# Kernel optimization log

Hardware: AMD Instinct MI355X
Metric: run time of the kernel (lower is better)

Reference implementation:

```python
import jax, jax.numpy as jnp
import numpy as np
import math

D = 768      # d_model
H = 12       # heads
DH = D // H  # per-head dim
HID = 3072   # ffn hidden
L = 6        # layers each for encoder/decoder
S = 1024     # encoder seq len
T = 1024     # decoder seq len
MAXLEN = 1024


def pos_encoding(d, length):
    # pe[pos, 2i] = sin(pos / scale**i), pe[pos, 2i+1] = cos(pos / scale**i), scale = 1000**(2/d)
    scale = 1000.0 ** (2.0 / d)
    inv = scale ** (-np.arange(d // 2, dtype=np.float64))
    ang = np.arange(length, dtype=np.float64)[:, None] * inv[None, :]
    pe = np.zeros((length, d), dtype=np.float32)
    pe[:, 0::2] = np.sin(ang)
    pe[:, 1::2] = np.cos(ang)
    return jnp.asarray(pe)


def setup_inputs() -> dict:
    key = jax.random.key(0)
    ks = iter(jax.random.split(key, 64))
    def nrm(shape, s=0.02):
        return jax.random.normal(next(ks), shape, dtype=jnp.float32) * s
    inp = {
        'xl': nrm((S, D), 1.0),
        'dl': nrm((T, D), 1.0),
        'pos_enc': pos_encoding(D, MAXLEN),
        # encoder params (stacked over L layers, heads stacked over H)
        'enc_wq': nrm((L, H, DH, D)), 'enc_wk': nrm((L, H, DH, D)), 'enc_wv': nrm((L, H, DH, D)),
        'enc_wo': nrm((L, D, D)), 'enc_bo': jnp.zeros((L, D), jnp.float32),
        'enc_ln_a': jnp.ones((L, 2, D), jnp.float32), 'enc_ln_b': jnp.zeros((L, 2, D), jnp.float32),
        'enc_w1': nrm((L, HID, D)), 'enc_b1': jnp.zeros((L, HID), jnp.float32),
        'enc_w2': nrm((L, D, HID)), 'enc_b2': jnp.zeros((L, D), jnp.float32),
        # decoder self-attention
        'dec_wq': nrm((L, H, DH, D)), 'dec_wk': nrm((L, H, DH, D)), 'dec_wv': nrm((L, H, DH, D)),
        'dec_wo': nrm((L, D, D)), 'dec_bo': jnp.zeros((L, D), jnp.float32),
        # decoder cross-attention
        'dec_cwq': nrm((L, H, DH, D)), 'dec_cwk': nrm((L, H, DH, D)), 'dec_cwv': nrm((L, H, DH, D)),
        'dec_cwo': nrm((L, D, D)), 'dec_cbo': jnp.zeros((L, D), jnp.float32),
        'dec_ln_a': jnp.ones((L, 3, D), jnp.float32), 'dec_ln_b': jnp.zeros((L, 3, D), jnp.float32),
        'dec_w1': nrm((L, HID, D)), 'dec_b1': jnp.zeros((L, HID), jnp.float32),
        'dec_w2': nrm((L, D, HID)), 'dec_b2': jnp.zeros((L, D), jnp.float32),
    }
    return inp


def _ln_res(x, fx, a, b, eps=1e-6):
    # x = x + fx; a*(x-mean)/(std+eps)+b with UNBIASED std (torch default) and std (not var) in denom
    x = x + fx
    m = x.mean(-1, keepdims=True)
    s = jnp.std(x, axis=-1, keepdims=True, ddof=1)
    return a * (x - m) / (s + eps) + b


def _mha(qx, kx, vx, wq, wk, wv, wo, bo, mask=None):
    q = jnp.einsum('sd,hed->hse', qx, wq)  # [H,S,dh]
    k = jnp.einsum('td,hed->hte', kx, wk)
    v = jnp.einsum('td,hed->hte', vx, wv)
    scores = jnp.einsum('hse,hte->hst', q, k) / math.sqrt(q.shape[-1])
    if mask is not None:
        scores = scores + mask
    p = jax.nn.softmax(scores, axis=-1)  # softmax over keys (torch dim=1 on 2D scores)
    o = jnp.einsum('hst,hte->hse', p, v)
    o = jnp.transpose(o, (1, 0, 2)).reshape(qx.shape[0], -1)  # concat heads
    return o @ wo.T + bo


def _ffn(x, w1, b1, w2, b2):
    return jax.nn.relu(x @ w1.T + b1) @ w2.T + b2


def reference(xl, dl, pos_enc, enc_wq, enc_wk, enc_wv, enc_wo, enc_bo, enc_ln_a, enc_ln_b,
              enc_w1, enc_b1, enc_w2, enc_b2,
              dec_wq, dec_wk, dec_wv, dec_wo, dec_bo,
              dec_cwq, dec_cwk, dec_cwv, dec_cwo, dec_cbo,
              dec_ln_a, dec_ln_b, dec_w1, dec_b1, dec_w2, dec_b2):
    m = xl + pos_enc[: xl.shape[0]]
    for l in range(L):
        fx = _mha(m, m, m, enc_wq[l], enc_wk[l], enc_wv[l], enc_wo[l], enc_bo[l])
        m = _ln_res(m, fx, enc_ln_a[l, 0], enc_ln_b[l, 0])
        fx = _ffn(m, enc_w1[l], enc_b1[l], enc_w2[l], enc_b2[l])
        m = _ln_res(m, fx, enc_ln_a[l, 1], enc_ln_b[l, 1])
    n = dl.shape[0]
    # additive causal mask: -10000 where j > i
    cmask = -10000.0 * (jnp.arange(n)[None, :] > jnp.arange(n)[:, None]).astype(jnp.float32)
    out = dl + pos_enc[:n]
    for l in range(L):
        fx = _mha(out, out, out, dec_wq[l], dec_wk[l], dec_wv[l], dec_wo[l], dec_bo[l], cmask)
        out = _ln_res(out, fx, dec_ln_a[l, 0], dec_ln_b[l, 0])
        fx = _mha(out, m, m, dec_cwq[l], dec_cwk[l], dec_cwv[l], dec_cwo[l], dec_cbo[l])
        out = _ln_res(out, fx, dec_ln_a[l, 1], dec_ln_b[l, 1])
        fx = _ffn(out, dec_w1[l], dec_b1[l], dec_w2[l], dec_b2[l])
        out = _ln_res(out, fx, dec_ln_a[l, 2], dec_ln_b[l, 2])
    return jax.nn.softmax(out, axis=1)
```

## Files before the change

### kernel.cpp

```cpp
#include <hip/hip_runtime.h>
#include <math.h>

#define DMODEL 768
#define NHEAD 12
#define DHEAD 64
#define HIDDEN 3072
#define NLAYER 6
#define SEQ 1024
#define AC_ELEMS (SEQ * DMODEL)

typedef unsigned short u16;
typedef __attribute__((ext_vector_type(8))) short short8;
typedef __attribute__((ext_vector_type(4))) float f32x4;

__device__ __forceinline__ u16 f2bf(float f) {
    union { float f; unsigned u; } v; v.f = f;
    unsigned u = v.u;
    return (u16)((u + 0x7fffu + ((u >> 16) & 1u)) >> 16);
}
__device__ __forceinline__ float bf2f(u16 b) {
    union { unsigned u; float f; } v; v.u = ((unsigned)b) << 16; return v.f;
}

__device__ __forceinline__ void async16(const void* g, void* l) {
    __builtin_amdgcn_global_load_lds(
        (const __attribute__((address_space(1))) unsigned int*)g,
        (__attribute__((address_space(3))) unsigned int*)l, 16, 0, 0);
}

__device__ __forceinline__ float block_sum(float v, float* red) {
    int tid = threadIdx.x;
    red[tid] = v;
    __syncthreads();
#pragma unroll
    for (int s = 128; s > 0; s >>= 1) {
        if (tid < s) red[tid] += red[tid + s];
        __syncthreads();
    }
    float r = red[0];
    __syncthreads();
    return r;
}
__device__ __forceinline__ float block_max(float v, float* red) {
    int tid = threadIdx.x;
    red[tid] = v;
    __syncthreads();
#pragma unroll
    for (int s = 128; s > 0; s >>= 1) {
        if (tid < s) red[tid] = fmaxf(red[tid], red[tid + s]);
        __syncthreads();
    }
    float r = red[0];
    __syncthreads();
    return r;
}

__global__ __launch_bounds__(256) void add_pe(const float* __restrict__ a,
                                              const float* __restrict__ b,
                                              float* __restrict__ o,
                                              u16* __restrict__ ob, int n) {
    int i = blockIdx.x * 256 + threadIdx.x;
    if (i < n) { float v = a[i] + b[i]; o[i] = v; ob[i] = f2bf(v); }
}

__global__ __launch_bounds__(256) void cvt_bf16(const float* __restrict__ src,
                                                u16* __restrict__ dst,
                                                long long per, long long sls, long long dls) {
    long long i = ((long long)blockIdx.x * 256 + threadIdx.x) * 4;
    if (i >= per) return;
    const float* s = src + (long long)blockIdx.y * sls + i;
    u16* d = dst + (long long)blockIdx.y * dls + i;
    float4 v = *(const float4*)s;
    ushort4 o;
    o.x = f2bf(v.x); o.y = f2bf(v.y); o.z = f2bf(v.z); o.w = f2bf(v.w);
    *(ushort4*)d = o;
}

template<int TM, int TN, int WR, int WC>
__global__ __launch_bounds__(WR * WC * 64) void gemm_mfma(
    const u16* __restrict__ A, int lda,
    const void* __restrict__ Bp, int ldb, int b_f32,
    const float* __restrict__ bias,
    void* __restrict__ Cp, int ldc, int c_bf16,
    float* __restrict__ C2,
    u16* __restrict__ vt_out, int vt_col0,
    int Ksub, int relu)
{
    constexpr int T  = WR * WC * 64;
    constexpr int FM = TM / (WR * 16), FN = TN / (WC * 16);
    constexpr int NA = TM * 8 / T, NB = TN * 8 / T;
    __shared__ __align__(16) u16 As[2][TM * 64];
    __shared__ __align__(16) u16 Bs[2][TN * 64];

    const int zs = blockIdx.z;
    const u16*   B16 = (const u16*)Bp   + (long long)zs * Ksub;
    const float* B32 = (const float*)Bp + (long long)zs * Ksub;
    A += (long long)zs * Ksub;
    u16*   C16 = (u16*)Cp;
    float* C32 = (float*)Cp;

    const int t = threadIdx.x, lane = t & 63, w = t >> 6;
    const int wy = w / WC, wx = w % WC;
    const int n0 = blockIdx.y * TM, m0 = blockIdx.x * TN;

    auto stage = [&](int b, int k0) {
#pragma unroll
        for (int i = 0; i < NA; ++i) {
            int L = i * T + t;
            int row = L >> 3, cp = L & 7, c = cp ^ (row & 7);
            async16(A + (long long)(n0 + row) * lda + k0 + (c << 3),
                    &As[b][(i * T + w * 64) * 8]);
        }
        if (!b_f32) {
#pragma unroll
            for (int i = 0; i < NB; ++i) {
                int L = i * T + t;
                int row = L >> 3, cp = L & 7, c = cp ^ (row & 7);
                async16(B16 + (long long)(m0 + row) * ldb + k0 + (c << 3),
                        &Bs[b][(i * T + w * 64) * 8]);
            }
        } else {
#pragma unroll
            for (int i = 0; i < NB; ++i) {
                int L = i * T + t;
                int row = L >> 3, cp = L & 7, c = cp ^ (row & 7);
                const float* s = B32 + (long long)(m0 + row) * ldb + k0 + (c << 3);
                float4 x = *(const float4*)s;
                float4 y = *(const float4*)(s + 4);
                uint4 pk;
                pk.x = (unsigned)f2bf(x.x) | ((unsigned)f2bf(x.y) << 16);
                pk.y = (unsigned)f2bf(x.z) | ((unsigned)f2bf(x.w) << 16);
                pk.z = (unsigned)f2bf(y.x) | ((unsigned)f2bf(y.y) << 16);
                pk.w = (unsigned)f2bf(y.z) | ((unsigned)f2bf(y.w) << 16);
                *(uint4*)&Bs[b][row * 64 + cp * 8] = pk;
            }
        }
    };

    const int nk = Ksub / 64;
    stage(0, 0);
    __syncthreads();

    f32x4 acc[FM][FN] = {};

    for (int tt = 0; tt < nk; ++tt) {
        const int cur = tt & 1;
        if (tt + 1 < nk) stage(cur ^ 1, (tt + 1) * 64);

        const u16* Ac = As[cur];
        const u16* Bc = Bs[cur];
#pragma unroll
        for (int kk = 0; kk < 2; ++kk) {
            short8 af[FM], bfv[FN];
            const int cb = kk * 4 + (lane >> 4);
#pragma unroll
            for (int m = 0; m < FM; ++m) {
                int R = wy * (TM / WR) + m * 16 + (lane & 15);
                af[m] = *(const short8*)&Ac[R * 64 + ((cb ^ (R & 7)) << 3)];
            }
#pragma unroll
            for (int n = 0; n < FN; ++n) {
                int R = wx * (TN / WC) + n * 16 + (lane & 15);
                bfv[n] = *(const short8*)&Bc[R * 64 + ((cb ^ (R & 7)) << 3)];
            }
#pragma unroll
            for (int m = 0; m < FM; ++m)
#pragma unroll
                for (int n = 0; n < FN; ++n)
                    acc[m][n] = __builtin_amdgcn_mfma_f32_16x16x32_bf16(af[m], bfv[n], acc[m][n], 0, 0, 0);
        }
        __syncthreads();
    }

    const int cj = lane & 15, ci0 = (lane >> 4) << 2;
    const bool z0 = (zs == 0);
#pragma unroll
    for (int m = 0; m < FM; ++m) {
#pragma unroll
        for (int n = 0; n < FN; ++n) {
            int col = m0 + wx * (TN / WC) + n * 16 + cj;
            bool to_vt = z0 && vt_out && (col >= vt_col0);
            float bv = (z0 && bias) ? bias[col] : 0.0f;
#pragma unroll
            for (int r = 0; r < 4; ++r) {
                int row = n0 + wy * (TM / WR) + m * 16 + ci0 + r;
                float v = acc[m][n][r] + bv;
                if (relu) v = fmaxf(v, 0.0f);
                if (!z0)          C2[(long long)row * ldc + col] = v;
                else if (to_vt)   vt_out[(long long)(col - vt_col0) * SEQ + row] = f2bf(v);
                else if (c_bf16)  C16[(long long)row * ldc + col] = f2bf(v);
                else              C32[(long long)row * ldc + col] = v;
            }
        }
    }
}

template<int CAUSAL>
__global__ __launch_bounds__(256) void attn_split(
    const u16* __restrict__ Qg,
    const u16* __restrict__ Kg,
    const u16* __restrict__ VT,
    float* __restrict__ Op,
    float* __restrict__ Ml)
{
    const int h  = blockIdx.y;
    const int qt = blockIdx.x;
    const int s  = blockIdx.z;
    const int q0 = qt * 64;
    const int t = threadIdx.x, lane = t & 63, w = t >> 6;

    const int last = CAUSAL ? qt : (SEQ / 64 - 1);

    if (CAUSAL && s > last) {
        for (int e = t; e < 64 * 64; e += 256) {
            int r = e >> 6, c = e & 63;
            Op[(long long)s * AC_ELEMS + (long long)(q0 + r) * DMODEL + h * 64 + c] = 0.0f;
        }
        if (t < 64) {
            long long mi = (((long long)s * NHEAD + h) * SEQ + q0 + t) * 2;
            Ml[mi] = -3.0e38f; Ml[mi + 1] = 0.0f;
        }
        return;
    }

    __shared__ __align__(16) u16 Ks[2][64 * 64];
    __shared__ __align__(16) u16 Vs[2][64 * 64];
    __shared__ __align__(16) u16 Ps[4][16 * 64];

    short8 qf[2];
    {
        int qrow = q0 + w * 16 + (lane & 15);
        const u16* qp = Qg + (long long)qrow * (3 * DMODEL) + h * DHEAD + ((lane >> 4) << 3);
        qf[0] = *(const short8*)qp;
        qf[1] = *(const short8*)(qp + 32);
    }

    auto stage = [&](int b, int kt) {
#pragma unroll
        for (int i = 0; i < 2; ++i) {
            int LL = i * 256 + t;
            int row = LL >> 3, cp = LL & 7, c = cp ^ (row & 7);
            async16(Kg + (long long)(kt * 64 + row) * (3 * DMODEL) + h * DHEAD + (c << 3),
                    &Ks[b][(i * 256 + w * 64) * 8]);
            async16(VT + (long long)(h * DHEAD + row) * SEQ + kt * 64 + (c << 3),
                    &Vs[b][(i * 256 + w * 64) * 8]);
        }
    };

    f32x4 o_acc[4] = {};
    float m_r[4], l_r[4];
#pragma unroll
    for (int r = 0; r < 4; ++r) { m_r[r] = -3.0e38f; l_r[r] = 0.f; }

    stage(0, s);
    __syncthreads();

    int buf = 0;
    for (int kt = s; kt <= last; kt += 2) {
        if (kt + 2 <= last) stage(buf ^ 1, kt + 2);

        f32x4 sv[4] = {};
#pragma unroll
        for (int kk = 0; kk < 2; ++kk) {
            const int cb = kk * 4 + (lane >> 4);
#pragma unroll
            for (int n = 0; n < 4; ++n) {
                int R = n * 16 + (lane & 15);
                short8 kf = *(const short8*)&Ks[buf][R * 64 + ((cb ^ (R & 7)) << 3)];
                sv[n] = __builtin_amdgcn_mfma_f32_16x16x32_bf16(qf[kk], kf, sv[n], 0, 0, 0);
            }
        }

#pragma unroll
        for (int n = 0; n < 4; ++n) {
            int keyl = n * 16 + (lane & 15);
#pragma unroll
            for (int r = 0; r < 4; ++r) {
                float v = sv[n][r] * 0.125f;
                if (CAUSAL && kt == qt) {
                    int ql = w * 16 + ((lane >> 4) << 2) + r;
                    if (keyl > ql) v -= 10000.0f;
                }
                sv[n][r] = v;
            }
        }

#pragma unroll
        for (int r = 0; r < 4; ++r) {
            float vm = fmaxf(fmaxf(sv[0][r], sv[1][r]), fmaxf(sv[2][r], sv[3][r]));
            vm = fmaxf(vm, __shfl_xor(vm, 1));
            vm = fmaxf(vm, __shfl_xor(vm, 2));
            vm = fmaxf(vm, __shfl_xor(vm, 4));
            vm = fmaxf(vm, __shfl_xor(vm, 8));
            float mn = fmaxf(m_r[r], vm);
            float sf = __expf(m_r[r] - mn);
            m_r[r] = mn;
            float rowsum = 0.f;
#pragma unroll
            for (int n = 0; n < 4; ++n) {
                float p = __expf(sv[n][r] - mn);
                sv[n][r] = p;
                rowsum += p;
            }
            rowsum += __shfl_xor(rowsum, 1);
            rowsum += __shfl_xor(rowsum, 2);
            rowsum += __shfl_xor(rowsum, 4);
            rowsum += __shfl_xor(rowsum, 8);
            l_r[r] = l_r[r] * sf + rowsum;
#pragma unroll
            for (int d = 0; d < 4; ++d) o_acc[d][r] *= sf;
        }

#pragma unroll
        for (int n = 0; n < 4; ++n) {
            int jh = lane & 7;
            int chunk = n * 2 + ((lane & 15) >> 3);
#pragma unroll
            for (int r = 0; r < 4; ++r) {
                int q = ((lane >> 4) << 2) + r;
                Ps[w][q * 64 + ((chunk ^ (q & 7)) << 3) + jh] = f2bf(sv[n][r]);
            }
        }

#pragma unroll
        for (int kk = 0; kk < 2; ++kk) {
            int q = lane & 15;
            int chunk = (lane >> 4) + kk * 4;
            short8 pf = *(const short8*)&Ps[w][q * 64 + ((chunk ^ (q & 7)) << 3)];
            const int cb = kk * 4 + (lane >> 4);
#pragma unroll
            for (int d = 0; d < 4; ++d) {
                int R = d * 16 + (lane & 15);
                short8 vf = *(const short8*)&Vs[buf][R * 64 + ((cb ^ (R & 7)) << 3)];
                o_acc[d] = __builtin_amdgcn_mfma_f32_16x16x32_bf16(pf, vf, o_acc[d], 0, 0, 0);
            }
        }
        __syncthreads();
        buf ^= 1;
    }

#pragma unroll
    for (int r = 0; r < 4; ++r) {
        int row = q0 + w * 16 + ((lane >> 4) << 2) + r;
#pragma unroll
        for (int d = 0; d < 4; ++d) {
            int col = h * DHEAD + d * 16 + (lane & 15);
            Op[(long long)s * AC_ELEMS + (long long)row * DMODEL + col] = o_acc[d][r];
        }
        if ((lane & 15) == 0) {
            long long mi = (((long long)s * NHEAD + h) * SEQ + row) * 2;
            Ml[mi] = m_r[r]; Ml[mi + 1] = l_r[r];
        }
    }
}

__global__ __launch_bounds__(192) void attn_combine(const float* __restrict__ Op,
                                                    const float* __restrict__ Ml,
                                                    u16* __restrict__ O) {
    const int row = blockIdx.x;
    const int c0 = threadIdx.x * 4;
    const int h = c0 >> 6;
    long long m0i = (((long long)0 * NHEAD + h) * SEQ + row) * 2;
    long long m1i = (((long long)1 * NHEAD + h) * SEQ + row) * 2;
    float m0 = Ml[m0i], l0 = Ml[m0i + 1];
    float m1 = Ml[m1i], l1 = Ml[m1i + 1];
    float M = fmaxf(m0, m1);
    float w0 = __expf(m0 - M), w1 = __expf(m1 - M);
    float inv = 1.0f / (w0 * l0 + w1 * l1);
    float4 a = *(const float4*)&Op[(long long)row * DMODEL + c0];
    float4 b = *(const float4*)&Op[(long long)AC_ELEMS + (long long)row * DMODEL + c0];
    ushort4 o;
    o.x = f2bf((w0 * a.x + w1 * b.x) * inv);
    o.y = f2bf((w0 * a.y + w1 * b.y) * inv);
    o.z = f2bf((w0 * a.z + w1 * b.z) * inv);
    o.w = f2bf((w0 * a.w + w1 * b.w) * inv);
    *(ushort4*)&O[(long long)row * DMODEL + c0] = o;
}

__global__ __launch_bounds__(256) void softmax_f32(const float* __restrict__ in,
                                                   float* __restrict__ out, int width) {
    const float* row = in + (long long)blockIdx.x * width;
    float* orow = out + (long long)blockIdx.x * width;
    int tid = threadIdx.x;
    __shared__ float red[256];
    int nf4 = width >> 2;
    float4 v = {-1e30f, -1e30f, -1e30f, -1e30f};
    if (tid < nf4) v = ((const float4*)row)[tid];
    float mx = fmaxf(fmaxf(v.x, v.y), fmaxf(v.z, v.w));
    mx = block_max(mx, red);
    float4 e = {0.f, 0.f, 0.f, 0.f};
    float s = 0.f;
    if (tid < nf4) {
        e.x = __expf(v.x - mx); e.y = __expf(v.y - mx);
        e.z = __expf(v.z - mx); e.w = __expf(v.w - mx);
        s = e.x + e.y + e.z + e.w;
    }
    s = block_sum(s, red);
    float inv = 1.0f / s;
    if (tid < nf4) {
        e.x *= inv; e.y *= inv; e.z *= inv; e.w *= inv;
        ((float4*)orow)[tid] = e;
    }
}

__global__ __launch_bounds__(256) void ln_res_kernel(float* __restrict__ x,
                                                     const float* __restrict__ fx,
                                                     const float* __restrict__ fx2,
                                                     const float* __restrict__ ga,
                                                     const float* __restrict__ gb,
                                                     u16* __restrict__ xb) {
    long long row = blockIdx.x;
    float* xr = x + row * DMODEL;
    const float* fr = fx + row * DMODEL;
    u16* xbr = xb + row * DMODEL;
    int tid = threadIdx.x;
    __shared__ float red[256];

    float4 tv = {0.f, 0.f, 0.f, 0.f};
    if (tid < 192) {
        float4 a = ((const float4*)xr)[tid];
        float4 f = ((const float4*)fr)[tid];
        tv.x = a.x + f.x; tv.y = a.y + f.y; tv.z = a.z + f.z; tv.w = a.w + f.w;
        if (fx2) {
            float4 g = ((const float4*)(fx2 + row * DMODEL))[tid];
            tv.x += g.x; tv.y += g.y; tv.z += g.z; tv.w += g.w;
        }
    }
    float sum = tv.x + tv.y + tv.z + tv.w;
    sum = block_sum(sum, red);
    float mean = sum * (1.0f / (float)DMODEL);

    float4 d = {0.f, 0.f, 0.f, 0.f};
    float ss = 0.f;
    if (tid < 192) {
        d.x = tv.x - mean; d.y = tv.y - mean; d.z = tv.z - mean; d.w = tv.w - mean;
        ss = d.x * d.x + d.y * d.y + d.z * d.z + d.w * d.w;
    }
    ss = block_sum(ss, red);
    float stdv = sqrtf(ss / (float)(DMODEL - 1));
    float inv = 1.0f / (stdv + 1e-6f);

    if (tid < 192) {
        float4 A = ((const float4*)ga)[tid];
        float4 B = ((const float4*)gb)[tid];
        float4 o;
        o.x = A.x * d.x * inv + B.x;
        o.y = A.y * d.y * inv + B.y;
        o.z = A.z * d.z * inv + B.z;
        o.w = A.w * d.w * inv + B.w;
        ((float4*)xr)[tid] = o;
        ushort4 ob;
        ob.x = f2bf(o.x); ob.y = f2bf(o.y); ob.z = f2bf(o.z); ob.w = f2bf(o.w);
        ((ushort4*)xbr)[tid] = ob;
    }
}

struct GArg {
    const u16* A; int lda;
    const void* B; int ldb; int b_f32;
    const float* bias;
    void* C; int ldc; int c_bf16;
    u16* vt; int vt_col0;
    int N, M, K; int relu;
};
template<int TM, int TN, int WR, int WC>
static inline void glaunch(hipStream_t st, const GArg& a, int splitk = 1, float* C2 = nullptr) {
    dim3 grid(a.M / TN, a.N / TM, splitk);
    hipLaunchKernelGGL((gemm_mfma<TM, TN, WR, WC>), grid, dim3(WR * WC * 64), 0, st,
                       a.A, a.lda, a.B, a.ldb, a.b_f32, a.bias, a.C, a.ldc, a.c_bf16,
                       C2, a.vt, a.vt_col0, a.K / splitk, a.relu);
}

extern "C" void kernel_launch(void* const* d_in, const int* in_sizes, int n_in,
                              void* d_out, int out_size, void* d_ws, size_t ws_size,
                              hipStream_t stream) {
    const float* xl      = (const float*)d_in[0];
    const float* dl      = (const float*)d_in[1];
    const float* pe      = (const float*)d_in[2];
    const float* enc_wq  = (const float*)d_in[3];
    const float* enc_wk  = (const float*)d_in[4];
    const float* enc_wv  = (const float*)d_in[5];
    const float* enc_wo  = (const float*)d_in[6];
    const float* enc_bo  = (const float*)d_in[7];
    const float* enc_lna = (const float*)d_in[8];
    const float* enc_lnb = (const float*)d_in[9];
    const float* enc_w1  = (const float*)d_in[10];
    const float* enc_b1  = (const float*)d_in[11];
    const float* enc_w2  = (const float*)d_in[12];
    const float* enc_b2  = (const float*)d_in[13];
    const float* dec_wq  = (const float*)d_in[14];
    const float* dec_wk  = (const float*)d_in[15];
    const float* dec_wv  = (const float*)d_in[16];
    const float* dec_wo  = (const float*)d_in[17];
    const float* dec_bo  = (const float*)d_in[18];
    const float* dec_cwq = (const float*)d_in[19];
    const float* dec_cwk = (const float*)d_in[20];
    const float* dec_cwv = (const float*)d_in[21];
    const float* dec_cwo = (const float*)d_in[22];
    const float* dec_cbo = (const float*)d_in[23];
    const float* dec_lna = (const float*)d_in[24];
    const float* dec_lnb = (const float*)d_in[25];
    const float* dec_w1  = (const float*)d_in[26];
    const float* dec_b1  = (const float*)d_in[27];
    const float* dec_w2  = (const float*)d_in[28];
    const float* dec_b2  = (const float*)d_in[29];

    const long long AC   = AC_ELEMS;
    const long long DD   = (long long)DMODEL * DMODEL;
    const long long WH   = (long long)HIDDEN * DMODEL;
    const long long QKVC = (long long)SEQ * 3 * DMODEL;
    const long long SH   = (long long)SEQ * HIDDEN;

    float* mbuf  = (float*)d_ws;
    float* xbuf  = mbuf + AC;
    float* fbuf  = xbuf + AC;
    float* fbuf2 = fbuf + AC;
    float* Opart = fbuf2 + AC;
    float* Ml    = Opart + 2 * AC;
    u16* u = (u16*)(Ml + 2LL * NHEAD * SEQ * 2);
    u16* mb16 = u;  u += AC;
    u16* xb16 = u;  u += AC;
    u16* qkvb = u;  u += QKVC;
    u16* vt   = u;  u += AC;
    u16* ob   = u;  u += AC;
    u16* hb   = u;  u += SH;

    u16* W = u;
    long long woff = 0;
    const long long W_ENC_QKV = woff; woff += 18 * DD;
    const long long W_ENC_WO  = woff; woff += 6 * DD;
    const long long W_ENC_W1  = woff; woff += 6 * WH;
    const long long W_ENC_W2  = woff; woff += 6 * WH;
    const long long W_DEC_QKV = woff; woff += 18 * DD;
    const long long W_DEC_CQKV= woff; woff += 18 * DD;
    const long long W_DEC_WO  = woff; woff += 6 * DD;
    const long long W_DEC_CWO = woff; woff += 6 * DD;
    const long long W_DEC_W1  = woff; woff += 6 * WH;
    const long long W_DEC_W2  = woff; woff += 6 * WH;
    const long long need = (long long)((char*)(W + woff) - (char*)d_ws);
    const bool conv = ((long long)ws_size >= need);

    if (conv) {
        auto cvt = [&](const float* src, long long dst_off, long long per, long long sls, long long dls, int L) {
            dim3 grid((unsigned)((per / 4 + 255) / 256), L);
            hipLaunchKernelGGL(cvt_bf16, grid, dim3(256), 0, stream, src, W + dst_off, per, sls, dls);
        };
        cvt(enc_wq, W_ENC_QKV + 0 * DD, DD, DD, 3 * DD, NLAYER);
        cvt(enc_wk, W_ENC_QKV + 1 * DD, DD, DD, 3 * DD, NLAYER);
        cvt(enc_wv, W_ENC_QKV + 2 * DD, DD, DD, 3 * DD, NLAYER);
        cvt(enc_wo, W_ENC_WO, 6 * DD, 0, 0, 1);
        cvt(enc_w1, W_ENC_W1, 6 * WH, 0, 0, 1);
        cvt(enc_w2, W_ENC_W2, 6 * WH, 0, 0, 1);
        cvt(dec_wq, W_DEC_QKV + 0 * DD, DD, DD, 3 * DD, NLAYER);
        cvt(dec_wk, W_DEC_QKV + 1 * DD, DD, DD, 3 * DD, NLAYER);
        cvt(dec_wv, W_DEC_QKV + 2 * DD, DD, DD, 3 * DD, NLAYER);
        cvt(dec_cwq, W_DEC_CQKV + 0 * DD, DD, DD, 3 * DD, NLAYER);
        cvt(dec_cwk, W_DEC_CQKV + 1 * DD, DD, DD, 3 * DD, NLAYER);
        cvt(dec_cwv, W_DEC_CQKV + 2 * DD, DD, DD, 3 * DD, NLAYER);
        cvt(dec_wo, W_DEC_WO, 6 * DD, 0, 0, 1);
        cvt(dec_cwo, W_DEC_CWO, 6 * DD, 0, 0, 1);
        cvt(dec_w1, W_DEC_W1, 6 * WH, 0, 0, 1);
        cvt(dec_w2, W_DEC_W2, 6 * WH, 0, 0, 1);
    }

    hipLaunchKernelGGL(add_pe, dim3((int)(AC / 256)), dim3(256), 0, stream, xl, pe, mbuf, mb16, (int)AC);

    auto attn = [&](int causal) {
        dim3 grid(SEQ / 64, NHEAD, 2);
        if (causal)
            hipLaunchKernelGGL((attn_split<1>), grid, dim3(256), 0, stream,
                               qkvb, qkvb + DMODEL, vt, Opart, Ml);
        else
            hipLaunchKernelGGL((attn_split<0>), grid, dim3(256), 0, stream,
                               qkvb, qkvb + DMODEL, vt, Opart, Ml);
        hipLaunchKernelGGL(attn_combine, dim3(SEQ), dim3(192), 0, stream, Opart, Ml, ob);
    };

    for (int l = 0; l < NLAYER; ++l) {
        if (conv) {
            GArg qkv = { mb16, DMODEL, W + W_ENC_QKV + l * 3 * DD, DMODEL, 0, nullptr,
                         qkvb, 3 * DMODEL, 1, vt, 2 * DMODEL, SEQ, 3 * DMODEL, DMODEL, 0 };
            glaunch<64, 64, 2, 2>(stream, qkv);
        } else {
            const float* wps[3] = { enc_wq + l * DD, enc_wk + l * DD, enc_wv + l * DD };
            for (int j = 0; j < 3; ++j) {
                GArg a = { mb16, DMODEL, wps[j], DMODEL, 1, nullptr,
                           qkvb + j * DMODEL, 3 * DMODEL, 1,
                           (j == 2) ? vt : nullptr, 0, SEQ, DMODEL, DMODEL, 0 };
                glaunch<32, 32, 1, 1>(stream, a);
            }
        }
        attn(0);
        GArg wo = { ob, DMODEL,
                    conv ? (const void*)(W + W_ENC_WO + l * DD) : (const void*)(enc_wo + l * DD),
                    DMODEL, conv ? 0 : 1, enc_bo + (long long)l * DMODEL,
                    fbuf, DMODEL, 0, nullptr, 0, SEQ, DMODEL, DMODEL, 0 };
        glaunch<32, 32, 1, 1>(stream, wo);
        hipLaunchKernelGGL(ln_res_kernel, dim3(SEQ), dim3(256), 0, stream,
                           mbuf, fbuf, (const float*)nullptr,
                           enc_lna + (long long)(l * 2 + 0) * DMODEL,
                           enc_lnb + (long long)(l * 2 + 0) * DMODEL, mb16);
        GArg f1 = { mb16, DMODEL,
                    conv ? (const void*)(W + W_ENC_W1 + l * WH) : (const void*)(enc_w1 + l * WH),
                    DMODEL, conv ? 0 : 1, enc_b1 + (long long)l * HIDDEN,
                    hb, HIDDEN, 1, nullptr, 0, SEQ, HIDDEN, DMODEL, 1 };
        glaunch<64, 64, 2, 2>(stream, f1);
        GArg f2 = { hb, HIDDEN,
                    conv ? (const void*)(W + W_ENC_W2 + l * WH) : (const void*)(enc_w2 + l * WH),
                    HIDDEN, conv ? 0 : 1, enc_b2 + (long long)l * DMODEL,
                    fbuf, DMODEL, 0, nullptr, 0, SEQ, DMODEL, HIDDEN, 0 };
        glaunch<64, 64, 2, 2>(stream, f2, 2, fbuf2);
        hipLaunchKernelGGL(ln_res_kernel, dim3(SEQ), dim3(256), 0, stream,
                           mbuf, fbuf, fbuf2,
                           enc_lna + (long long)(l * 2 + 1) * DMODEL,
                           enc_lnb + (long long)(l * 2 + 1) * DMODEL, mb16);
    }

    hipLaunchKernelGGL(add_pe, dim3((int)(AC / 256)), dim3(256), 0, stream, dl, pe, xbuf, xb16, (int)AC);

    for (int l = 0; l < NLAYER; ++l) {
        if (conv) {
            GArg qkv = { xb16, DMODEL, W + W_DEC_QKV + l * 3 * DD, DMODEL, 0, nullptr,
                         qkvb, 3 * DMODEL, 1, vt, 2 * DMODEL, SEQ, 3 * DMODEL, DMODEL, 0 };
            glaunch<64, 64, 2, 2>(stream, qkv);
        } else {
            const float* wps[3] = { dec_wq + l * DD, dec_wk + l * DD, dec_wv + l * DD };
            for (int j = 0; j < 3; ++j) {
                GArg a = { xb16, DMODEL, wps[j], DMODEL, 1, nullptr,
                           qkvb + j * DMODEL, 3 * DMODEL, 1,
                           (j == 2) ? vt : nullptr, 0, SEQ, DMODEL, DMODEL, 0 };
                glaunch<32, 32, 1, 1>(stream, a);
            }
        }
        attn(1);
        GArg wo = { ob, DMODEL,
                    conv ? (const void*)(W + W_DEC_WO + l * DD) : (const void*)(dec_wo + l * DD),
                    DMODEL, conv ? 0 : 1, dec_bo + (long long)l * DMODEL,
                    fbuf, DMODEL, 0, nullptr, 0, SEQ, DMODEL, DMODEL, 0 };
        glaunch<32, 32, 1, 1>(stream, wo);
        hipLaunchKernelGGL(ln_res_kernel, dim3(SEQ), dim3(256), 0, stream,
                           xbuf, fbuf, (const float*)nullptr,
                           dec_lna + (long long)(l * 3 + 0) * DMODEL,
                           dec_lnb + (long long)(l * 3 + 0) * DMODEL, xb16);

        if (conv) {
            GArg q = { xb16, DMODEL, W + W_DEC_CQKV + l * 3 * DD, DMODEL, 0, nullptr,
                       qkvb, 3 * DMODEL, 1, nullptr, 0, SEQ, DMODEL, DMODEL, 0 };
            glaunch<32, 32, 1, 1>(stream, q);
            GArg kv = { mb16, DMODEL, W + W_DEC_CQKV + l * 3 * DD + DD, DMODEL, 0, nullptr,
                        qkvb + DMODEL, 3 * DMODEL, 1, vt, DMODEL, SEQ, 2 * DMODEL, DMODEL, 0 };
            glaunch<32, 32, 1, 1>(stream, kv);
        } else {
            GArg q = { xb16, DMODEL, dec_cwq + l * DD, DMODEL, 1, nullptr,
                       qkvb, 3 * DMODEL, 1, nullptr, 0, SEQ, DMODEL, DMODEL, 0 };
            glaunch<32, 32, 1, 1>(stream, q);
            GArg ck = { mb16, DMODEL, dec_cwk + l * DD, DMODEL, 1, nullptr,
                        qkvb + DMODEL, 3 * DMODEL, 1, nullptr, 0, SEQ, DMODEL, DMODEL, 0 };
            glaunch<32, 32, 1, 1>(stream, ck);
            GArg cv = { mb16, DMODEL, dec_cwv + l * DD, DMODEL, 1, nullptr,
                        qkvb + 2 * DMODEL, 3 * DMODEL, 1, vt, 0, SEQ, DMODEL, DMODEL, 0 };
            glaunch<32, 32, 1, 1>(stream, cv);
        }
        attn(0);
        GArg cwo = { ob, DMODEL,
                     conv ? (const void*)(W + W_DEC_CWO + l * DD) : (const void*)(dec_cwo + l * DD),
                     DMODEL, conv ? 0 : 1, dec_cbo + (long long)l * DMODEL,
                     fbuf, DMODEL, 0, nullptr, 0, SEQ, DMODEL, DMODEL, 0 };
        glaunch<32, 32, 1, 1>(stream, cwo);
        hipLaunchKernelGGL(ln_res_kernel, dim3(SEQ), dim3(256), 0, stream,
                           xbuf, fbuf, (const float*)nullptr,
                           dec_lna + (long long)(l * 3 + 1) * DMODEL,
                           dec_lnb + (long long)(l * 3 + 1) * DMODEL, xb16);

        GArg f1 = { xb16, DMODEL,
                    conv ? (const void*)(W + W_DEC_W1 + l * WH) : (const void*)(dec_w1 + l * WH),
                    DMODEL, conv ? 0 : 1, dec_b1 + (long long)l * HIDDEN,
                    hb, HIDDEN, 1, nullptr, 0, SEQ, HIDDEN, DMODEL, 1 };
        glaunch<64, 64, 2, 2>(stream, f1);
        GArg f2 = { hb, HIDDEN,
                    conv ? (const void*)(W + W_DEC_W2 + l * WH) : (const void*)(dec_w2 + l * WH),
                    HIDDEN, conv ? 0 : 1, dec_b2 + (long long)l * DMODEL,
                    fbuf, DMODEL, 0, nullptr, 0, SEQ, DMODEL, HIDDEN, 0 };
        glaunch<64, 64, 2, 2>(stream, f2, 2, fbuf2);
        hipLaunchKernelGGL(ln_res_kernel, dim3(SEQ), dim3(256), 0, stream,
                           xbuf, fbuf, fbuf2,
                           dec_lna + (long long)(l * 3 + 2) * DMODEL,
                           dec_lnb + (long long)(l * 3 + 2) * DMODEL, xb16);
    }

    hipLaunchKernelGGL(softmax_f32, dim3(SEQ), dim3(256), 0, stream, xbuf, (float*)d_out, DMODEL);
}
```

Before: 1.746 ms.

## Triple-buffer GEMM staging with counted vmcnt waits and leaner barriers

The GEMM moves from double to triple-buffered LDS staging, prefetching two K-tiles ahead. Full __syncthreads drains are replaced with explicit s_waitcnt vmcnt counts plus raw s_barrier, so async loads for later tiles can stay in flight. The attention kernel gets the same counted-wait scheme. This aims to hide global-to-LDS latency, but it raises LDS use, which can lower occupancy, and correctness now depends on the hand-counted outstanding-load numbers.

New measurement: 1.750 ms. No clear change (+0.3%).

```diff
diff --git a/kernel.cpp b/kernel.cpp
--- a/kernel.cpp
+++ b/kernel.cpp
@@ -26,6 +26,20 @@
     __builtin_amdgcn_global_load_lds(
         (const __attribute__((address_space(1))) unsigned int*)g,
         (__attribute__((address_space(3))) unsigned int*)l, 16, 0, 0);
+}
+
+template<int N> __device__ __forceinline__ void waitv() {
+    asm volatile("s_waitcnt vmcnt(%0)" :: "n"(N) : "memory");
+    __builtin_amdgcn_sched_barrier(0);
+}
+__device__ __forceinline__ void drain_all() {
+    asm volatile("s_waitcnt vmcnt(0) lgkmcnt(0)" ::: "memory");
+    __builtin_amdgcn_sched_barrier(0);
+}
+__device__ __forceinline__ void bar() {
+    __builtin_amdgcn_sched_barrier(0);
+    __builtin_amdgcn_s_barrier();
+    __builtin_amdgcn_sched_barrier(0);
 }
 
 __device__ __forceinline__ float block_sum(float v, float* red) {
@@ -87,10 +101,12 @@
     int Ksub, int relu)
 {
     constexpr int T  = WR * WC * 64;
+    constexpr bool MW = (WR * WC) > 1;
     constexpr int FM = TM / (WR * 16), FN = TN / (WC * 16);
     constexpr int NA = TM * 8 / T, NB = TN * 8 / T;
-    __shared__ __align__(16) u16 As[2][TM * 64];
-    __shared__ __align__(16) u16 Bs[2][TN * 64];
+    constexpr int LPS = NA + NB;
+    __shared__ __align__(16) u16 As[3][TM * 64];
+    __shared__ __align__(16) u16 Bs[3][TN * 64];
 
     const int zs = blockIdx.z;
     const u16*   B16 = (const u16*)Bp   + (long long)zs * Ksub;
@@ -139,16 +155,20 @@
 
     const int nk = Ksub / 64;
     stage(0, 0);
-    __syncthreads();
+    if (nk > 1) stage(1, 64);
 
     f32x4 acc[FM][FN] = {};
 
     for (int tt = 0; tt < nk; ++tt) {
-        const int cur = tt & 1;
-        if (tt + 1 < nk) stage(cur ^ 1, (tt + 1) * 64);
-
-        const u16* Ac = As[cur];
-        const u16* Bc = Bs[cur];
+        if (tt + 2 < nk) stage((tt + 2) % 3, (tt + 2) * 64);
+        if (b_f32)             drain_all();
+        else if (tt + 2 < nk)  waitv<2 * LPS>();
+        else if (tt + 1 < nk)  waitv<LPS>();
+        else                   waitv<0>();
+        if (MW) bar();
+
+        const u16* Ac = As[tt % 3];
+        const u16* Bc = Bs[tt % 3];
 #pragma unroll
         for (int kk = 0; kk < 2; ++kk) {
             short8 af[FM], bfv[FN];
@@ -169,7 +189,7 @@
                 for (int n = 0; n < FN; ++n)
                     acc[m][n] = __builtin_amdgcn_mfma_f32_16x16x32_bf16(af[m], bfv[n], acc[m][n], 0, 0, 0);
         }
-        __syncthreads();
+        if (MW) bar();
     }
 
     const int cj = lane & 15, ci0 = (lane >> 4) << 2;
@@ -253,11 +273,12 @@
     for (int r = 0; r < 4; ++r) { m_r[r] = -3.0e38f; l_r[r] = 0.f; }
 
     stage(0, s);
-    __syncthreads();
 
     int buf = 0;
     for (int kt = s; kt <= last; kt += 2) {
-        if (kt + 2 <= last) stage(buf ^ 1, kt + 2);
+        if (kt + 2 <= last) { stage(buf ^ 1, kt + 2); waitv<4>(); }
+        else                { waitv<0>(); }
+        bar();
 
         f32x4 sv[4] = {};
 #pragma unroll
@@ -335,7 +356,7 @@
                 o_acc[d] = __builtin_amdgcn_mfma_f32_16x16x32_bf16(pf, vf, o_acc[d], 0, 0, 0);
             }
         }
-        __syncthreads();
+        bar();
         buf ^= 1;
     }
 
```
